# Performance work log

Measured on AMD Instinct MI355X. Metric: run time of the kernel, lower is better.

Reference implementation:

```python
import jax, jax.numpy as jnp
import numpy as np

N_NODES = 100000
N_EDGES = 3200000
F_IN = 1433
HID = 16
N_CLS = 7


def setup_inputs() -> dict:
    key = jax.random.key(0)
    k1, k2, k3, k4 = jax.random.split(key, 4)
    x = jax.random.normal(k1, (N_NODES, F_IN), dtype=jnp.float32)
    edge_index = jax.random.randint(k2, (2, N_EDGES), 0, N_NODES, dtype=jnp.int32)
    # Glorot-style init like GCNConv
    W1 = jax.random.normal(k3, (F_IN, HID), dtype=jnp.float32) * (1.0 / np.sqrt(F_IN))
    b1 = jnp.zeros((HID,), dtype=jnp.float32)
    W2 = jax.random.normal(k4, (HID, N_CLS), dtype=jnp.float32) * (1.0 / np.sqrt(HID))
    b2 = jnp.zeros((N_CLS,), dtype=jnp.float32)
    return {"x": x, "edge_index": edge_index, "W1": W1, "b1": b1, "W2": W2, "b2": b2}


def _gcn_conv(h, src, dst, W, b):
    # GCNConv with normalize=False: dense transform, then unweighted sum-aggregate
    # over incoming edges plus a self-loop (add_self_loops=True default), then bias.
    t = h @ W                                   # [N, out]
    agg = jax.ops.segment_sum(t[src], dst, num_segments=N_NODES)  # scatter-add over edges
    return agg + t + b                          # '+ t' = self-loop contribution


def reference(x, edge_index, W1, b1, W2, b2):
    src, dst = edge_index[0], edge_index[1]
    h = jax.nn.relu(_gcn_conv(x, src, dst, W1, b1))
    # F.dropout(training=False) is identity in eval mode
    out = _gcn_conv(h, src, dst, W2, b2)
    return out
```

## Files before the change

### kernel.cpp

```cpp
#include <hip/hip_runtime.h>

#define N_NODES 100000
#define N_EDGES 3200000
#define F_IN    1433
#define HID     16
#define N_CLS   7
#define NWINT   48
#define NWIN    12
#define GB1     (N_NODES / 16)
#define QBLK    (N_EDGES / 4 / 256)
#define NTOT    ((long)N_NODES * F_IN)
#define NBKT    1024
#define NPBK    98
#define BCAP2   512
#define SRCM    0x1FFFF

typedef __attribute__((ext_vector_type(8))) short short8v;
typedef __attribute__((ext_vector_type(4))) float float4v;

typedef const __attribute__((address_space(1))) unsigned* gptr_t;
typedef __attribute__((address_space(3))) unsigned* lptr_t;

__device__ __forceinline__ unsigned short f2bf(float f) {
    unsigned u = __float_as_uint(f);
    u += 0x7fffu + ((u >> 16) & 1u);
    return (unsigned short)(u >> 16);
}

__device__ __forceinline__ void gll16(const float* g, float* lds) {
    gptr_t gp = (gptr_t)(unsigned long long)(uintptr_t)g;
    lptr_t lp = (lptr_t)(unsigned)(uintptr_t)lds;
    __builtin_amdgcn_global_load_lds(gp, lp, 16, 0, 0);
}

__global__ void prep_w1_kernel(const float* __restrict__ W1, short* __restrict__ w1f) {
    int w = blockIdx.x;
    int l = threadIdx.x;
    int col = l & 15;
    int kb = w * 32 + (l >> 4) * 8;
    short8v f;
#pragma unroll
    for (int i = 0; i < 8; ++i) {
        int k = kb + i;
        float v = (k < F_IN) ? W1[k * HID + col] : 0.f;
        f[i] = (short)f2bf(v);
    }
    *(short8v*)(w1f + ((size_t)w * 64 + l) * 8) = f;
}

__device__ __noinline__ void gemm_arm(int gid, const float* __restrict__ x,
                                      const short* __restrict__ w1f,
                                      float* __restrict__ t1) {
    __shared__ float xs[4][2][512];
    __shared__ float red[4][256];
    const int tid = threadIdx.x;
    const int s = tid >> 6;
    const int l = tid & 63;
    const int R0 = gid * 16;
    const int g = l >> 4;
    const int c = l & 15;
    const short* __restrict__ wfp = w1f + ((size_t)(s * NWIN) * 64 + l) * 8;

    short8v bf[NWIN];
#pragma unroll
    for (int wl = 0; wl < NWIN; ++wl)
        bf[wl] = *(const short8v*)(wfp + (size_t)wl * 512);

    const int lr = l >> 3;
    const int q = (l & 7) ^ lr;
    const long gb0 = (long)(R0 + lr) * F_IN + q * 4;
    const long gb1 = (long)(R0 + 8 + lr) * F_IN + q * 4;
    const bool last = (gid == GB1 - 1);
    const int kbase = s * NWIN * 32;

    const int p0f = (c * 8 + ((2 * g) ^ (c & 7))) * 16;
    const int p1  = (c * 8 + ((2 * g + 1) ^ (c & 7))) * 16;

    {
        long gi0 = gb0 + kbase, gi1 = gb1 + kbase;
        if (last) { if (gi0 > NTOT - 4) gi0 = NTOT - 4; if (gi1 > NTOT - 4) gi1 = NTOT - 4; }
        gll16(x + gi0, &xs[s][0][0]);
        gll16(x + gi1, &xs[s][0][256]);
    }

    float4v acc = {0.f, 0.f, 0.f, 0.f};
#pragma unroll
    for (int wl = 0; wl < NWIN; ++wl) {
        if (wl + 1 < NWIN) {
            int buf = (wl + 1) & 1;
            long kw = kbase + (long)(wl + 1) * 32;
            long gi0 = gb0 + kw, gi1 = gb1 + kw;
            if (last) { if (gi0 > NTOT - 4) gi0 = NTOT - 4; if (gi1 > NTOT - 4) gi1 = NTOT - 4; }
            gll16(x + gi0, &xs[s][buf][0]);
            gll16(x + gi1, &xs[s][buf][256]);
            asm volatile("s_waitcnt vmcnt(2)" ::: "memory");
        } else {
            asm volatile("s_waitcnt vmcnt(0)" ::: "memory");
        }
        __builtin_amdgcn_sched_barrier(0);
        const char* bb = (const char*)&xs[s][wl & 1][0];
        float4 lo = *(const float4*)(bb + p0f);
        float4 hi = *(const float4*)(bb + p1);
        short8v af;
        af[0] = (short)f2bf(lo.x); af[1] = (short)f2bf(lo.y);
        af[2] = (short)f2bf(lo.z); af[3] = (short)f2bf(lo.w);
        af[4] = (short)f2bf(hi.x); af[5] = (short)f2bf(hi.y);
        af[6] = (short)f2bf(hi.z); af[7] = (short)f2bf(hi.w);
        acc = __builtin_amdgcn_mfma_f32_16x16x32_bf16(af, bf[wl], acc, 0, 0, 0);
    }

#pragma unroll
    for (int j = 0; j < 4; ++j) red[s][l * 4 + j] = acc[j];
    __syncthreads();
    {
        int r = tid >> 4, cc = tid & 15;
        int idx = ((r >> 2) * 16 + cc) * 4 + (r & 3);
        float vv = red[0][idx] + red[1][idx] + red[2][idx] + red[3][idx];
        t1[(long)(R0 + r) * HID + cc] = vv;
    }
}

__device__ __noinline__ void fill_arm(int fbid, const int* __restrict__ src,
                                      const int* __restrict__ dst,
                                      int* __restrict__ cnt, int* __restrict__ bkt) {
    const int p = blockIdx.x & 7;
    int i = fbid * 256 + threadIdx.x;
    int4 s4 = ((const int4*)src)[i];
    int4 d4 = ((const int4*)dst)[i];
    unsigned b, dl; int pos;
    b = (unsigned)d4.x / NPBK; dl = (unsigned)d4.x - b * NPBK;
    pos = atomicAdd(&cnt[(p << 10) + b], 1);
    if (pos < BCAP2) bkt[((size_t)((p << 10) + b) << 9) + pos] = (int)((dl << 17) | (unsigned)s4.x);
    b = (unsigned)d4.y / NPBK; dl = (unsigned)d4.y - b * NPBK;
    pos = atomicAdd(&cnt[(p << 10) + b], 1);
    if (pos < BCAP2) bkt[((size_t)((p << 10) + b) << 9) + pos] = (int)((dl << 17) | (unsigned)s4.y);
    b = (unsigned)d4.z / NPBK; dl = (unsigned)d4.z - b * NPBK;
    pos = atomicAdd(&cnt[(p << 10) + b], 1);
    if (pos < BCAP2) bkt[((size_t)((p << 10) + b) << 9) + pos] = (int)((dl << 17) | (unsigned)s4.z);
    b = (unsigned)d4.w / NPBK; dl = (unsigned)d4.w - b * NPBK;
    pos = atomicAdd(&cnt[(p << 10) + b], 1);
    if (pos < BCAP2) bkt[((size_t)((p << 10) + b) << 9) + pos] = (int)((dl << 17) | (unsigned)s4.w);
}

__global__ __launch_bounds__(256) void fat1_kernel(const float* __restrict__ x,
                                                   const short* __restrict__ w1f,
                                                   float* __restrict__ t1,
                                                   const int* __restrict__ src,
                                                   const int* __restrict__ dst,
                                                   int* __restrict__ cnt,
                                                   int* __restrict__ bkt) {
    const int bid = blockIdx.x;
    if (bid % 3 == 2) fill_arm((bid - 2) / 3, src, dst, cnt, bkt);
    else              gemm_arm(bid - (bid + 1) / 3, x, w1f, t1);
}

__global__ __launch_bounds__(256) void agg1f_kernel(const float* __restrict__ t1,
                                                    const int* __restrict__ cnt,
                                                    const int* __restrict__ bkt,
                                                    const float* __restrict__ b1,
                                                    const float* __restrict__ W2,
                                                    float* __restrict__ t2p) {
    __shared__ int els[4096];
    __shared__ int ecsr[4096];
    __shared__ int dcnt[128], doff[128], dcur[128];
    __shared__ int pbase[9];
    __shared__ float hl[NPBK][16];
    const int b = blockIdx.x;
    const int t = threadIdx.x;
    if (t == 0) {
        int s = 0;
        for (int p = 0; p < 8; ++p) {
            pbase[p] = s;
            int ne = cnt[(p << 10) + b]; if (ne > BCAP2) ne = BCAP2;
            s += ne;
        }
        pbase[8] = s;
    }
    if (t < 128) dcnt[t] = 0;
    __syncthreads();
    const int nt = pbase[8];
    for (int p = 0; p < 8; ++p) {
        int base0 = pbase[p], ne = pbase[p + 1] - base0;
        const int* __restrict__ bp = bkt + ((size_t)((p << 10) + b) << 9);
        for (int e = t; e < ne; e += 256) els[base0 + e] = bp[e];
    }
    __syncthreads();
    for (int e = t; e < nt; e += 256) atomicAdd(&dcnt[els[e] >> 17], 1);
    __syncthreads();
    if (t < 128) doff[t] = dcnt[t];
    __syncthreads();
    for (int d = 1; d < 128; d <<= 1) {
        int add = (t < 128 && t >= d) ? doff[t - d] : 0;
        __syncthreads();
        if (t < 128) doff[t] += add;
        __syncthreads();
    }
    if (t < 128) dcur[t] = doff[t] - dcnt[t];
    __syncthreads();
    for (int e = t; e < nt; e += 256) {
        int v = els[e];
        int pos = atomicAdd(&dcur[v >> 17], 1);
        ecsr[pos] = v & SRCM;
    }
    __syncthreads();
    const int nbase = b * NPBK;
    {
        int q = t & 3;
        for (int nl = t >> 2; nl < NPBK; nl += 64) {
            int node = nbase + nl;
            if (node < N_NODES) {
                int o = doff[nl] - dcnt[nl];
                int d = dcnt[nl];
                float4 a = *(const float4*)(t1 + ((size_t)node * 16 + q * 4));
                float4 bb = *(const float4*)(b1 + q * 4);
                a.x += bb.x; a.y += bb.y; a.z += bb.z; a.w += bb.w;
                for (int e = 0; e < d; ++e) {
                    int s = ecsr[o + e];
                    float4 v = *(const float4*)(t1 + ((size_t)s * 16 + q * 4));
                    a.x += v.x; a.y += v.y; a.z += v.z; a.w += v.w;
                }
                float4 r = {fmaxf(a.x, 0.f), fmaxf(a.y, 0.f),
                            fmaxf(a.z, 0.f), fmaxf(a.w, 0.f)};
                *(float4*)(&hl[nl][q * 4]) = r;
            }
        }
    }
    __syncthreads();
    for (int idx = t; idx < NPBK * 8; idx += 256) {
        int ln = idx >> 3, c = idx & 7;
        int node = nbase + ln;
        if (node < N_NODES) {
            float a = 0.f;
            if (c < N_CLS) {
#pragma unroll
                for (int j = 0; j < HID; ++j) a = fmaf(hl[ln][j], W2[j * N_CLS + c], a);
            }
            t2p[(size_t)node * 8 + c] = a;
        }
    }
}

__global__ __launch_bounds__(256) void agg2_kernel(const float* __restrict__ t2p,
                                                   const int* __restrict__ cnt,
                                                   const int* __restrict__ bkt,
                                                   const float* __restrict__ b2,
                                                   float* __restrict__ out) {
    __shared__ int els[4096];
    __shared__ int ecsr[4096];
    __shared__ int dcnt[128], doff[128], dcur[128];
    __shared__ int pbase[9];
    const int b = blockIdx.x;
    const int t = threadIdx.x;
    if (t == 0) {
        int s = 0;
        for (int p = 0; p < 8; ++p) {
            pbase[p] = s;
            int ne = cnt[(p << 10) + b]; if (ne > BCAP2) ne = BCAP2;
            s += ne;
        }
        pbase[8] = s;
    }
    if (t < 128) dcnt[t] = 0;
    __syncthreads();
    const int nt = pbase[8];
    for (int p = 0; p < 8; ++p) {
        int base0 = pbase[p], ne = pbase[p + 1] - base0;
        const int* __restrict__ bp = bkt + ((size_t)((p << 10) + b) << 9);
        for (int e = t; e < ne; e += 256) els[base0 + e] = bp[e];
    }
    __syncthreads();
    for (int e = t; e < nt; e += 256) atomicAdd(&dcnt[els[e] >> 17], 1);
    __syncthreads();
    if (t < 128) doff[t] = dcnt[t];
    __syncthreads();
    for (int d = 1; d < 128; d <<= 1) {
        int add = (t < 128 && t >= d) ? doff[t - d] : 0;
        __syncthreads();
        if (t < 128) doff[t] += add;
        __syncthreads();
    }
    if (t < 128) dcur[t] = doff[t] - dcnt[t];
    __syncthreads();
    for (int e = t; e < nt; e += 256) {
        int v = els[e];
        int pos = atomicAdd(&dcur[v >> 17], 1);
        ecsr[pos] = v & SRCM;
    }
    __syncthreads();
    const int nbase = b * NPBK;
    {
        int q = t & 1;
        for (int nl = t >> 1; nl < NPBK; nl += 128) {
            int node = nbase + nl;
            if (node < N_NODES) {
                int o = doff[nl] - dcnt[nl];
                int d = dcnt[nl];
                float4 a = *(const float4*)(t2p + ((size_t)node * 8 + q * 4));
                if (q == 0) {
                    a.x += b2[0]; a.y += b2[1]; a.z += b2[2]; a.w += b2[3];
                } else {
                    a.x += b2[4]; a.y += b2[5]; a.z += b2[6];
                }
                for (int e = 0; e < d; ++e) {
                    int s = ecsr[o + e];
                    float4 v = *(const float4*)(t2p + ((size_t)s * 8 + q * 4));
                    a.x += v.x; a.y += v.y; a.z += v.z; a.w += v.w;
                }
                float* op = out + (size_t)node * 7 + q * 4;
                op[0] = a.x; op[1] = a.y; op[2] = a.z;
                if (q == 0) op[3] = a.w;
            }
        }
    }
}


extern "C" void kernel_launch(void* const* d_in, const int* in_sizes, int n_in,
                              void* d_out, int out_size, void* d_ws, size_t ws_size,
                              hipStream_t stream) {
    const float* x  = (const float*)d_in[0];
    const int*   ei = (const int*)d_in[1];
    const float* W1 = (const float*)d_in[2];
    const float* b1 = (const float*)d_in[3];
    const float* W2 = (const float*)d_in[4];
    const float* b2 = (const float*)d_in[5];
    const int* src = ei;
    const int* dst = ei + N_EDGES;
    float* out = (float*)d_out;

    char* w = (char*)d_ws;
    float* t1  = (float*)w;  w += (size_t)N_NODES * HID * sizeof(float);
    float* t2p = (float*)w;  w += (size_t)N_NODES * 8 * sizeof(float);
    short* w1f = (short*)w;  w += (size_t)NWINT * 64 * 8 * sizeof(short);
    int* cnt   = (int*)w;    w += (size_t)8 * NBKT * sizeof(int);
    int* bkt   = (int*)w;    w += (size_t)8 * NBKT * BCAP2 * sizeof(int);

    (void)hipMemsetAsync(cnt, 0, (size_t)8 * NBKT * sizeof(int), stream);
    prep_w1_kernel<<<NWINT, 64, 0, stream>>>(W1, w1f);

    fat1_kernel<<<GB1 + QBLK, 256, 0, stream>>>(x, w1f, t1, src, dst, cnt, bkt);

    agg1f_kernel<<<NBKT, 256, 0, stream>>>(t1, cnt, bkt, b1, W2, t2p);
    agg2_kernel<<<NBKT, 256, 0, stream>>>(t2p, cnt, bkt, b2, out);
}
```

Before: 287.9 us.

## Load x cooperatively in wide per-row K phases with block-shared triple buffering

Before, each wave streamed its own contiguous K segment of 16 rows in 32-float windows. Now all four waves together fetch 16 rows by 128 floats per phase, into a three-stage shared buffer synchronised with a block barrier, and each wave takes an interleaved 32-wide K slice of each phase. This gives longer contiguous global reads per row and frees LDS by reusing the stage buffer for the final cross-wave reduction. In exchange it adds a block-wide barrier every phase, which couples the waves and may stall on the slowest one.

After: 286.6 us. No clear change (-0.5%).

```diff
diff --git a/kernel.cpp b/kernel.cpp
--- a/kernel.cpp
+++ b/kernel.cpp
@@ -6,7 +6,6 @@
 #define HID     16
 #define N_CLS   7
 #define NWINT   48
-#define NWIN    12
 #define GB1     (N_NODES / 16)
 #define QBLK    (N_EDGES / 4 / 256)
 #define NTOT    ((long)N_NODES * F_IN)
@@ -51,71 +50,69 @@
 __device__ __noinline__ void gemm_arm(int gid, const float* __restrict__ x,
                                       const short* __restrict__ w1f,
                                       float* __restrict__ t1) {
-    __shared__ float xs[4][2][512];
-    __shared__ float red[4][256];
+    __shared__ float xs[3][16][128];
     const int tid = threadIdx.x;
     const int s = tid >> 6;
     const int l = tid & 63;
     const int R0 = gid * 16;
     const int g = l >> 4;
     const int c = l & 15;
-    const short* __restrict__ wfp = w1f + ((size_t)(s * NWIN) * 64 + l) * 8;
-
-    short8v bf[NWIN];
-#pragma unroll
-    for (int wl = 0; wl < NWIN; ++wl)
-        bf[wl] = *(const short8v*)(wfp + (size_t)wl * 512);
-
-    const int lr = l >> 3;
-    const int q = (l & 7) ^ lr;
-    const long gb0 = (long)(R0 + lr) * F_IN + q * 4;
-    const long gb1 = (long)(R0 + 8 + lr) * F_IN + q * 4;
+
+    short8v bf[12];
+#pragma unroll
+    for (int ph = 0; ph < 12; ++ph)
+        bf[ph] = *(const short8v*)(w1f + ((size_t)((ph * 4 + s) * 64 + l)) * 8);
+
+    const int row_a = 2 * s + (l >> 5);
+    const int cs = l & 31;
     const bool last = (gid == GB1 - 1);
-    const int kbase = s * NWIN * 32;
-
-    const int p0f = (c * 8 + ((2 * g) ^ (c & 7))) * 16;
-    const int p1  = (c * 8 + ((2 * g + 1) ^ (c & 7))) * 16;
-
-    {
-        long gi0 = gb0 + kbase, gi1 = gb1 + kbase;
-        if (last) { if (gi0 > NTOT - 4) gi0 = NTOT - 4; if (gi1 > NTOT - 4) gi1 = NTOT - 4; }
-        gll16(x + gi0, &xs[s][0][0]);
-        gll16(x + gi1, &xs[s][0][256]);
-    }
+
+#define ISSUE(ph_)                                                              \
+    {                                                                           \
+        _Pragma("unroll")                                                       \
+        for (int i = 0; i < 2; ++i) {                                           \
+            int row = i * 8 + row_a;                                            \
+            int gch = cs ^ (row & 7);                                           \
+            long gi = (long)(R0 + row) * F_IN + (ph_) * 128 + gch * 4;          \
+            if (last && gi > NTOT - 4) gi = NTOT - 4;                           \
+            gll16(x + gi, &xs[(ph_) % 3][i * 8 + 2 * s][0]);                    \
+        }                                                                       \
+    }
+
+    ISSUE(0); ISSUE(1);
+
+    const int p0 = ((s * 8 + 2 * g) ^ (c & 7)) * 4;
+    const int p1 = ((s * 8 + 2 * g + 1) ^ (c & 7)) * 4;
 
     float4v acc = {0.f, 0.f, 0.f, 0.f};
 #pragma unroll
-    for (int wl = 0; wl < NWIN; ++wl) {
-        if (wl + 1 < NWIN) {
-            int buf = (wl + 1) & 1;
-            long kw = kbase + (long)(wl + 1) * 32;
-            long gi0 = gb0 + kw, gi1 = gb1 + kw;
-            if (last) { if (gi0 > NTOT - 4) gi0 = NTOT - 4; if (gi1 > NTOT - 4) gi1 = NTOT - 4; }
-            gll16(x + gi0, &xs[s][buf][0]);
-            gll16(x + gi1, &xs[s][buf][256]);
-            asm volatile("s_waitcnt vmcnt(2)" ::: "memory");
-        } else {
-            asm volatile("s_waitcnt vmcnt(0)" ::: "memory");
-        }
+    for (int ph = 0; ph < 12; ++ph) {
+        if (ph < 11) asm volatile("s_waitcnt vmcnt(2)" ::: "memory");
+        else         asm volatile("s_waitcnt vmcnt(0)" ::: "memory");
         __builtin_amdgcn_sched_barrier(0);
-        const char* bb = (const char*)&xs[s][wl & 1][0];
-        float4 lo = *(const float4*)(bb + p0f);
-        float4 hi = *(const float4*)(bb + p1);
+        __builtin_amdgcn_s_barrier();
+        if (ph + 2 < 12) ISSUE(ph + 2);
+        const float* rowp = &xs[ph % 3][c][0];
+        float4 lo = *(const float4*)(rowp + p0);
+        float4 hi = *(const float4*)(rowp + p1);
         short8v af;
         af[0] = (short)f2bf(lo.x); af[1] = (short)f2bf(lo.y);
         af[2] = (short)f2bf(lo.z); af[3] = (short)f2bf(lo.w);
         af[4] = (short)f2bf(hi.x); af[5] = (short)f2bf(hi.y);
         af[6] = (short)f2bf(hi.z); af[7] = (short)f2bf(hi.w);
-        acc = __builtin_amdgcn_mfma_f32_16x16x32_bf16(af, bf[wl], acc, 0, 0, 0);
-    }
-
-#pragma unroll
-    for (int j = 0; j < 4; ++j) red[s][l * 4 + j] = acc[j];
+        acc = __builtin_amdgcn_mfma_f32_16x16x32_bf16(af, bf[ph], acc, 0, 0, 0);
+    }
+#undef ISSUE
+
+    float* reds = &xs[0][0][0] + s * 256;
+#pragma unroll
+    for (int j = 0; j < 4; ++j) reds[l * 4 + j] = acc[j];
     __syncthreads();
     {
         int r = tid >> 4, cc = tid & 15;
         int idx = ((r >> 2) * 16 + cc) * 4 + (r & 3);
-        float vv = red[0][idx] + red[1][idx] + red[2][idx] + red[3][idx];
+        float* rb = &xs[0][0][0];
+        float vv = rb[idx] + rb[256 + idx] + rb[512 + idx] + rb[768 + idx];
         t1[(long)(R0 + r) * HID + cc] = vv;
     }
 }
```
